# Kernel optimization log

Measured on AMD Instinct MI355X. Metric: run time of the kernel, lower is better.

Reference implementation:

```python
import jax, jax.numpy as jnp
import numpy as np

D = 256
EXP = 4


def layer_norm(x, gamma, beta, eps=1e-5):
    mu = jnp.mean(x, axis=-1, keepdims=True)
    var = jnp.var(x, axis=-1, keepdims=True)
    return (x - mu) / jnp.sqrt(var + eps) * gamma + beta


def setup_inputs() -> dict:
    key = jax.random.key(0)
    ks = jax.random.split(key, 7)
    B, N = 8, 2048
    x = jax.random.normal(ks[0], (B, N, D), dtype=jnp.float32)
    w1 = jax.random.normal(ks[1], (D, EXP * D), dtype=jnp.float32) * (1.0 / np.sqrt(D))
    b1 = jnp.zeros((EXP * D,), dtype=jnp.float32)
    w2 = jax.random.normal(ks[2], (EXP * D, D), dtype=jnp.float32) * (1.0 / np.sqrt(EXP * D))
    b2 = jnp.zeros((D,), dtype=jnp.float32)
    g1 = jnp.ones((D,), dtype=jnp.float32)
    be1 = jnp.zeros((D,), dtype=jnp.float32)
    g2 = jnp.ones((D,), dtype=jnp.float32)
    be2 = jnp.zeros((D,), dtype=jnp.float32)
    return {"x": x, "w1": w1, "b1": b1, "w2": w2, "b2": b2,
            "gamma1": g1, "beta1": be1, "gamma2": g2, "beta2": be2}


def reference(x, w1, b1, w2, b2, gamma1, beta1, gamma2, beta2):
    # Sublayer 1: x + SA(LN(x)); SA uses raw QK^T softmax with Q=K=V=LN(x)
    h = layer_norm(x, gamma1, beta1)               # [B,N,D]
    scale = jnp.sqrt(jnp.float32(h.shape[-1]))
    scores = jnp.einsum('bnd,bmd->bnm', h, h) / scale  # [B,N,N]
    prob = jax.nn.softmax(scores, axis=-1)
    sa_out = jnp.einsum('bnm,bmd->bnd', prob, h)
    x = x + sa_out
    # Sublayer 2: x + FFN(LN(x))
    h2 = layer_norm(x, gamma2, beta2)
    ffn = jax.nn.relu(h2 @ w1 + b1) @ w2 + b2
    return x + ffn
```

## Files before the change

kernel.cpp:

```cpp
#include <hip/hip_runtime.h>
#include <hip/hip_bf16.h>

typedef unsigned short u16;
typedef unsigned int u32;
typedef __attribute__((ext_vector_type(8))) short short8;
typedef __attribute__((ext_vector_type(4))) short short4v;
typedef __attribute__((ext_vector_type(4))) float f32x4;

typedef unsigned int __attribute__((address_space(1))) as1_u32;
typedef unsigned int __attribute__((address_space(3))) as3_u32;

__device__ __forceinline__ void gload16(const void* g, void* l) {
    __builtin_amdgcn_global_load_lds((const as1_u32*)g, (as3_u32*)l, 16, 0, 0);
}

__device__ __forceinline__ u16 f2b(float f) {
    union { float f; unsigned u; } v; v.f = f;
    unsigned r = v.u + 0x7fffu + ((v.u >> 16) & 1u);
    return (u16)(r >> 16);
}

__device__ __forceinline__ f32x4 mfma32(short8 a, short8 b, f32x4 c) {
    return __builtin_amdgcn_mfma_f32_16x16x32_bf16(a, b, c, 0, 0, 0);
}
__device__ __forceinline__ f32x4 mfma16(short4v a, short4v b, f32x4 c) {
    asm("v_mfma_f32_16x16x16_bf16 %0, %1, %2, %0" : "+v"(c) : "v"(a), "v"(b));
    return c;
}

__global__ void transpose_cast(const float* __restrict__ src,
                               u16* __restrict__ dst, int R, int C) {
    __shared__ float tile[32][33];
    const int c0 = blockIdx.x * 32, r0 = blockIdx.y * 32;
    const int tx = threadIdx.x, ty = threadIdx.y;
#pragma unroll
    for (int i = ty; i < 32; i += 8)
        tile[i][tx] = src[(size_t)(r0 + i) * C + c0 + tx];
    __syncthreads();
#pragma unroll
    for (int i = ty; i < 32; i += 8)
        dst[(size_t)(c0 + i) * R + r0 + tx] = f2b(tile[tx][i]);
}

__global__ void transpose_bf16(const u16* __restrict__ src, u16* __restrict__ dst) {
    __shared__ u16 t[32][33];
    const int b = blockIdx.z;
    const int n0 = blockIdx.x * 32, d0 = blockIdx.y * 32;
    const int tx = threadIdx.x, ty = threadIdx.y;
    const u16* s = src + (size_t)b * (2048 * 256);
    u16* d = dst + (size_t)b * (2048 * 256);
#pragma unroll
    for (int i = ty; i < 32; i += 8)
        t[i][tx] = s[(size_t)(n0 + i) * 256 + d0 + tx];
    __syncthreads();
#pragma unroll
    for (int i = ty; i < 32; i += 8)
        d[(size_t)(d0 + i) * 2048 + n0 + tx] = t[tx][i];
}

__global__ __launch_bounds__(256) void ln_kernel(
    const float* __restrict__ x, const float* __restrict__ g,
    const float* __restrict__ be, u16* __restrict__ out) {
    const int lane = threadIdx.x & 63;
    const size_t row = (size_t)blockIdx.x * 4 + (threadIdx.x >> 6);
    const float4 v = *((const float4*)(x + row * 256) + lane);
    float s  = v.x + v.y + v.z + v.w;
    float s2 = v.x * v.x + v.y * v.y + v.z * v.z + v.w * v.w;
#pragma unroll
    for (int m = 1; m < 64; m <<= 1) {
        s  += __shfl_xor(s, m);
        s2 += __shfl_xor(s2, m);
    }
    const float mean = s * (1.0f / 256.0f);
    const float var  = s2 * (1.0f / 256.0f) - mean * mean;
    const float rstd = rsqrtf(var + 1e-5f);
    const float4 gv = *((const float4*)g + lane);
    const float4 bv = *((const float4*)be + lane);
    ushort4 o;
    o.x = f2b((v.x - mean) * rstd * gv.x + bv.x);
    o.y = f2b((v.y - mean) * rstd * gv.y + bv.y);
    o.z = f2b((v.z - mean) * rstd * gv.z + bv.z);
    o.w = f2b((v.w - mean) * rstd * gv.w + bv.w);
    *((ushort4*)(out + row * 256) + lane) = o;
}

#define ATTN_LDS_BYTES (2*65536 + 2048)

__global__ __launch_bounds__(512, 2) void attn_kernel(
    const u16* __restrict__ h, const u16* __restrict__ hT,
    const float* __restrict__ x, float* __restrict__ xmid) {
    extern __shared__ char smem[];
    const int tid  = threadIdx.x;
    const int w    = tid >> 6;
    const int lane = tid & 63;
    const int grp  = lane >> 4;
    const int l16  = lane & 15;
    const int kvq  = w & 3;
    const int qh   = w >> 2;
    const int bid  = blockIdx.x;
    const int b    = bid & 7;
    const int q0   = (bid >> 3) * 64;

    const u16* hb = h + (size_t)b * (2048 * 256);
    const char* hbB = (const char*)hb;
    const char* hTB = (const char*)(hT + (size_t)b * (2048 * 256));

    short8 qf[2][8];
#pragma unroll
    for (int st = 0; st < 2; ++st) {
        const u16* qp = hb + (size_t)(q0 + qh * 32 + st * 16 + l16) * 256 + grp * 8;
#pragma unroll
        for (int kk = 0; kk < 8; ++kk) qf[st][kk] = *(const short8*)(qp + kk * 32);
    }

    f32x4 oacc[2][16];
#pragma unroll
    for (int st = 0; st < 2; ++st)
#pragma unroll
        for (int dt = 0; dt < 16; ++dt) oacc[st][dt] = (f32x4){0.f, 0.f, 0.f, 0.f};
    float m_run[2] = {-1e30f, -1e30f};
    float l_run[2] = {0.f, 0.f};

    const char* gK0 = hbB + ((size_t)(tid >> 5) << 9)
                          + (((tid & 31) ^ ((tid >> 5) & 7)) << 4);
    const char* gV0 = hTB + ((size_t)(tid >> 3) << 12)
                          + (((tid & 7) ^ ((tid >> 3) & 7)) << 4);

    {
        char* lK = smem + w * 1024;
        char* lV = smem + 32768 + w * 1024;
#pragma unroll
        for (int it = 0; it < 4; ++it) gload16(gK0 + (size_t)it * 8192, lK + it * 8192);
#pragma unroll
        for (int it = 0; it < 4; ++it) gload16(gV0 + (size_t)it * 262144, lV + it * 8192);
    }
    __syncthreads();

    for (int kt = 0; kt < 32; ++kt) {
        const int cur = kt & 1;
        if (kt < 31) {
            char* lK = smem + (cur ^ 1) * 65536 + w * 1024;
            char* lV = smem + (cur ^ 1) * 65536 + 32768 + w * 1024;
            const char* gK = gK0 + (size_t)(kt + 1) * 32768;
            const char* gV = gV0 + (size_t)(kt + 1) * 128;
#pragma unroll
            for (int it = 0; it < 4; ++it) gload16(gK + (size_t)it * 8192, lK + it * 8192);
#pragma unroll
            for (int it = 0; it < 4; ++it) gload16(gV + (size_t)it * 262144, lV + it * 8192);
        }
        const char* KB = smem + cur * 65536;
        const char* VB = KB + 32768;

        f32x4 sacc[2] = {(f32x4){0.f,0.f,0.f,0.f}, (f32x4){0.f,0.f,0.f,0.f}};
        const char* rb = KB + ((kvq * 16 + l16) << 9);
#pragma unroll
        for (int kk = 0; kk < 8; ++kk) {
            const int c = grp + 4 * kk;
            const int swz = (c & ~7) | ((c ^ l16) & 7);
            const short8 kf = *(const short8*)(rb + (swz << 4));
            sacc[0] = mfma32(kf, qf[0][kk], sacc[0]);
            sacc[1] = mfma32(kf, qf[1][kk], sacc[1]);
        }

        short4v pa[2];
#pragma unroll
        for (int st = 0; st < 2; ++st) {
            float p0 = sacc[st][0] * 0.0625f, p1 = sacc[st][1] * 0.0625f;
            float p2 = sacc[st][2] * 0.0625f, p3 = sacc[st][3] * 0.0625f;
            float mx = fmaxf(fmaxf(p0, p1), fmaxf(p2, p3));
            mx = fmaxf(mx, __shfl_xor(mx, 16));
            mx = fmaxf(mx, __shfl_xor(mx, 32));
            if (__any(mx > m_run[st] + 8.f)) {
                const float mnew  = fmaxf(m_run[st], mx);
                const float alpha = __expf(m_run[st] - mnew);
                m_run[st] = mnew;
                l_run[st] *= alpha;
                float ar[4];
#pragma unroll
                for (int r = 0; r < 4; ++r) ar[r] = __shfl(alpha, grp * 4 + r);
#pragma unroll
                for (int dt = 0; dt < 16; ++dt)
#pragma unroll
                    for (int r = 0; r < 4; ++r) oacc[st][dt][r] *= ar[r];
            }
            const float e0 = __expf(p0 - m_run[st]);
            const float e1 = __expf(p1 - m_run[st]);
            const float e2 = __expf(p2 - m_run[st]);
            const float e3 = __expf(p3 - m_run[st]);
            float lt = e0 + e1 + e2 + e3;
            lt += __shfl_xor(lt, 16);
            lt += __shfl_xor(lt, 32);
            l_run[st] += lt;
            pa[st] = (short4v){(short)f2b(e0), (short)f2b(e1),
                               (short)f2b(e2), (short)f2b(e3)};
        }

        const char* vbase = VB + l16 * 128
                          + (((kvq * 2 + (grp >> 1)) ^ (l16 & 7)) << 4)
                          + (grp & 1) * 8;
#pragma unroll
        for (int dt = 0; dt < 16; ++dt) {
            const short4v bv = *(const short4v*)(vbase + dt * 2048);
            oacc[0][dt] = mfma16(pa[0], bv, oacc[0][dt]);
            oacc[1][dt] = mfma16(pa[1], bv, oacc[1][dt]);
        }
        __syncthreads();
    }

    float2* ml = (float2*)(smem + 131072);
    if (lane < 16) {
        float2 t0; t0.x = m_run[0]; t0.y = l_run[0];
        float2 t1; t1.x = m_run[1]; t1.y = l_run[1];
        ml[w * 32 + lane]      = t0;
        ml[w * 32 + 16 + lane] = t1;
    }
    const int dq = w & 3;
    float an[2][4][4];
    const float* xb = x + (size_t)b * (2048 * 256);
    float* ob = xmid + (size_t)b * (2048 * 256);
#pragma unroll
    for (int rnd = 0; rnd < 2; ++rnd) {
        char* wb = smem + w * 16384;
#pragma unroll
        for (int st = 0; st < 2; ++st)
#pragma unroll
            for (int k = 0; k < 8; ++k)
                *(f32x4*)(wb + ((st * 8 + k) * 64 + lane) * 16) = oacc[st][rnd * 8 + k];
        __syncthreads();
        if (rnd == 0) {
#pragma unroll
            for (int st = 0; st < 2; ++st)
#pragma unroll
                for (int rr = 0; rr < 4; ++rr) {
                    const int q = st * 16 + grp * 4 + rr;
                    float mv[4], lv[4];
#pragma unroll
                    for (int kq = 0; kq < 4; ++kq) {
                        const float2 t = ml[(qh * 4 + kq) * 32 + q];
                        mv[kq] = t.x; lv[kq] = t.y;
                    }
                    const float M = fmaxf(fmaxf(mv[0], mv[1]), fmaxf(mv[2], mv[3]));
                    float a[4], L = 0.f;
#pragma unroll
                    for (int kq = 0; kq < 4; ++kq) {
                        a[kq] = __expf(mv[kq] - M);
                        L += a[kq] * lv[kq];
                    }
                    const float inv = 1.0f / L;
#pragma unroll
                    for (int kq = 0; kq < 4; ++kq) an[st][rr][kq] = a[kq] * inv;
                }
        }
#pragma unroll
        for (int j = 0; j < 2; ++j) {
            const int dtg = rnd * 8 + dq * 2 + j;
#pragma unroll
            for (int st = 0; st < 2; ++st) {
                f32x4 acc = (f32x4){0.f, 0.f, 0.f, 0.f};
#pragma unroll
                for (int kq = 0; kq < 4; ++kq) {
                    const f32x4 ch = *(const f32x4*)(smem + (qh * 4 + kq) * 16384
                                     + ((st * 8 + dq * 2 + j) * 64 + lane) * 16);
#pragma unroll
                    for (int rr = 0; rr < 4; ++rr) acc[rr] += an[st][rr][kq] * ch[rr];
                }
                const int col = dtg * 16 + l16;
#pragma unroll
                for (int rr = 0; rr < 4; ++rr) {
                    const int row = q0 + qh * 32 + st * 16 + grp * 4 + rr;
                    const size_t idx = (size_t)row * 256 + col;
                    ob[idx] = xb[idx] + acc[rr];
                }
            }
        }
        if (rnd == 0) __syncthreads();
    }
}

#define FFN_LDS_BYTES (2*65536 + 4096)

__global__ __launch_bounds__(512, 2) void ffn_kernel(
    const u16* __restrict__ h2, const u16* __restrict__ w1t,
    const u16* __restrict__ w2t, const float* __restrict__ b1,
    const float* __restrict__ b2, float* __restrict__ xmid) {
    extern __shared__ char smem[];
    const int tid  = threadIdx.x;
    const int w    = tid >> 6;
    const int lane = tid & 63;
    const int grp  = lane >> 4;
    const int l16  = lane & 15;
    const int hq   = w & 3;
    const int th   = w >> 2;
    const int t0   = blockIdx.x * 64;
    char* b1lds = smem + 131072;

    short8 af[2][8];
#pragma unroll
    for (int st = 0; st < 2; ++st) {
        const u16* ap = h2 + (size_t)(t0 + th * 32 + st * 16 + l16) * 256 + grp * 8;
#pragma unroll
        for (int kk = 0; kk < 8; ++kk) af[st][kk] = *(const short8*)(ap + kk * 32);
    }

    f32x4 oacc[2][16];
#pragma unroll
    for (int st = 0; st < 2; ++st)
#pragma unroll
        for (int dt = 0; dt < 16; ++dt) oacc[st][dt] = (f32x4){0.f, 0.f, 0.f, 0.f};

    const char* g10 = (const char*)w1t + ((size_t)(tid >> 5) << 9)
                                       + (((tid & 31) ^ ((tid >> 5) & 7)) << 4);
    const char* g20 = (const char*)w2t + ((size_t)(tid >> 3) << 11)
                                       + (((tid & 7) ^ ((tid >> 3) & 7)) << 4);

    {
        char* l1 = smem + w * 1024;
        char* l2 = smem + 32768 + w * 1024;
#pragma unroll
        for (int it = 0; it < 4; ++it) gload16(g10 + (size_t)it * 8192, l1 + it * 8192);
#pragma unroll
        for (int it = 0; it < 4; ++it) gload16(g20 + (size_t)it * 131072, l2 + it * 8192);
        if (tid < 256) gload16((const char*)b1 + tid * 16, b1lds + tid * 16);
    }
    __syncthreads();

    for (int hc = 0; hc < 16; ++hc) {
        const int cur = hc & 1;
        if (hc < 15) {
            char* l1 = smem + (cur ^ 1) * 65536 + w * 1024;
            char* l2 = smem + (cur ^ 1) * 65536 + 32768 + w * 1024;
            const char* g1 = g10 + (size_t)(hc + 1) * 32768;
            const char* g2 = g20 + (size_t)(hc + 1) * 128;
#pragma unroll
            for (int it = 0; it < 4; ++it) gload16(g1 + (size_t)it * 8192, l1 + it * 8192);
#pragma unroll
            for (int it = 0; it < 4; ++it) gload16(g2 + (size_t)it * 131072, l2 + it * 8192);
        }
        const char* W1B = smem + cur * 65536;
        const char* W2B = W1B + 32768;

        f32x4 sacc[2] = {(f32x4){0.f,0.f,0.f,0.f}, (f32x4){0.f,0.f,0.f,0.f}};
        const char* rb = W1B + ((hq * 16 + l16) << 9);
#pragma unroll
        for (int kk = 0; kk < 8; ++kk) {
            const int c = grp + 4 * kk;
            const int swz = (c & ~7) | ((c ^ l16) & 7);
            const short8 wf = *(const short8*)(rb + (swz << 4));
            sacc[0] = mfma32(wf, af[0][kk], sacc[0]);
            sacc[1] = mfma32(wf, af[1][kk], sacc[1]);
        }

        const f32x4 bb = *(const f32x4*)(b1lds + (hc * 64 + hq * 16 + grp * 4) * 4);
        short4v pa[2];
#pragma unroll
        for (int st = 0; st < 2; ++st) {
            const float v0 = fmaxf(sacc[st][0] + bb[0], 0.f);
            const float v1 = fmaxf(sacc[st][1] + bb[1], 0.f);
            const float v2 = fmaxf(sacc[st][2] + bb[2], 0.f);
            const float v3 = fmaxf(sacc[st][3] + bb[3], 0.f);
            pa[st] = (short4v){(short)f2b(v0), (short)f2b(v1),
                               (short)f2b(v2), (short)f2b(v3)};
        }

        const char* vbase = W2B + l16 * 128
                          + (((hq * 2 + (grp >> 1)) ^ (l16 & 7)) << 4)
                          + (grp & 1) * 8;
#pragma unroll
        for (int dt = 0; dt < 16; ++dt) {
            const short4v bv = *(const short4v*)(vbase + dt * 2048);
            oacc[0][dt] = mfma16(pa[0], bv, oacc[0][dt]);
            oacc[1][dt] = mfma16(pa[1], bv, oacc[1][dt]);
        }
        __syncthreads();
    }

    const int dq = w & 3;
#pragma unroll
    for (int rnd = 0; rnd < 2; ++rnd) {
        char* wb = smem + w * 16384;
#pragma unroll
        for (int st = 0; st < 2; ++st)
#pragma unroll
            for (int k = 0; k < 8; ++k)
                *(f32x4*)(wb + ((st * 8 + k) * 64 + lane) * 16) = oacc[st][rnd * 8 + k];
        __syncthreads();
#pragma unroll
        for (int j = 0; j < 2; ++j) {
            const int dtg = rnd * 8 + dq * 2 + j;
            const int col = dtg * 16 + l16;
            const float b2v = b2[col];
#pragma unroll
            for (int st = 0; st < 2; ++st) {
                f32x4 acc = (f32x4){0.f, 0.f, 0.f, 0.f};
#pragma unroll
                for (int kq = 0; kq < 4; ++kq) {
                    const f32x4 ch = *(const f32x4*)(smem + (th * 4 + kq) * 16384
                                     + ((st * 8 + dq * 2 + j) * 64 + lane) * 16);
#pragma unroll
                    for (int rr = 0; rr < 4; ++rr) acc[rr] += ch[rr];
                }
#pragma unroll
                for (int rr = 0; rr < 4; ++rr) {
                    const int row = t0 + th * 32 + st * 16 + grp * 4 + rr;
                    const size_t idx = (size_t)row * 256 + col;
                    xmid[idx] = xmid[idx] + acc[rr] + b2v;
                }
            }
        }
        if (rnd == 0) __syncthreads();
    }
}

extern "C" void kernel_launch(void* const* d_in, const int* in_sizes, int n_in,
                              void* d_out, int out_size, void* d_ws, size_t ws_size,
                              hipStream_t stream) {
    (void)in_sizes; (void)n_in; (void)out_size; (void)ws_size;
    const float* x   = (const float*)d_in[0];
    const float* w1  = (const float*)d_in[1];
    const float* b1  = (const float*)d_in[2];
    const float* w2  = (const float*)d_in[3];
    const float* b2  = (const float*)d_in[4];
    const float* g1  = (const float*)d_in[5];
    const float* be1 = (const float*)d_in[6];
    const float* g2  = (const float*)d_in[7];
    const float* be2 = (const float*)d_in[8];
    float* out = (float*)d_out;

    char* ws = (char*)d_ws;
    u16* h   = (u16*)ws;
    u16* hT  = (u16*)(ws + 8388608);
    u16* w1t = (u16*)(ws + 16777216);
    u16* w2t = (u16*)(ws + 17301504);

    hipFuncSetAttribute((const void*)attn_kernel,
                        hipFuncAttributeMaxDynamicSharedMemorySize, ATTN_LDS_BYTES);
    hipFuncSetAttribute((const void*)ffn_kernel,
                        hipFuncAttributeMaxDynamicSharedMemorySize, FFN_LDS_BYTES);

    transpose_cast<<<dim3(32, 8), dim3(32, 8), 0, stream>>>(w1, w1t, 256, 1024);
    transpose_cast<<<dim3(8, 32), dim3(32, 8), 0, stream>>>(w2, w2t, 1024, 256);

    ln_kernel<<<4096, 256, 0, stream>>>(x, g1, be1, h);
    transpose_bf16<<<dim3(64, 8, 8), dim3(32, 8), 0, stream>>>(h, hT);
    attn_kernel<<<256, 512, ATTN_LDS_BYTES, stream>>>(h, hT, x, out);

    ln_kernel<<<4096, 256, 0, stream>>>(out, g2, be2, h);
    ffn_kernel<<<256, 512, FFN_LDS_BYTES, stream>>>(h, w1t, w2t, b1, b2, out);
}
```

Baseline: 199.0 us.

## Pre-pack V and W2 into MFMA-ready tiled layout with contiguous loads and setprio

Replaces the plain transposes of h and W2 with packing kernels that write each 64-row tile as a contiguous, pre-swizzled 32KB block. Attention and FFN kernels can then stream V/W2 tiles with contiguous 16-byte global-to-LDS loads instead of strided ones. They also read one short8 per lane to feed two 16x16x16 MFMAs, halving the LDS read count. s_setprio is raised around the MFMA loops to favour matrix issue across waves. This adds more intricate index arithmetic in the packers, which could introduce layout bugs.

```diff
diff --git a/kernel.cpp b/kernel.cpp
--- a/kernel.cpp
+++ b/kernel.cpp
@@ -42,20 +42,58 @@
         dst[(size_t)(c0 + i) * R + r0 + tx] = f2b(tile[tx][i]);
 }
 
-__global__ void transpose_bf16(const u16* __restrict__ src, u16* __restrict__ dst) {
+__global__ void pack_v(const u16* __restrict__ h, u16* __restrict__ hV) {
     __shared__ u16 t[32][33];
     const int b = blockIdx.z;
     const int n0 = blockIdx.x * 32, d0 = blockIdx.y * 32;
     const int tx = threadIdx.x, ty = threadIdx.y;
-    const u16* s = src + (size_t)b * (2048 * 256);
-    u16* d = dst + (size_t)b * (2048 * 256);
+    const u16* s = h + (size_t)b * (2048 * 256);
 #pragma unroll
     for (int i = ty; i < 32; i += 8)
         t[i][tx] = s[(size_t)(n0 + i) * 256 + d0 + tx];
     __syncthreads();
+    const int tid = ty * 32 + tx;
+    if (tid < 128) {
+        const int kvc = tid & 7, dl = tid >> 3;
+        short8 vv;
+#pragma unroll
+        for (int e = 0; e < 4; ++e) {
+            vv[e]     = (short)t[kvc * 4 + e][dl];
+            vv[4 + e] = (short)t[kvc * 4 + e][dl + 16];
+        }
+        const int kt   = n0 >> 6;
+        const int kv4  = ((n0 & 32) >> 2) + kvc;
+        const int slot = (d0 >> 5) ^ (dl & 7);
+        char* dst = (char*)hV + ((size_t)b * 32 + kt) * 32768
+                  + (kv4 * 16 + dl) * 128 + slot * 16;
+        *(short8*)dst = vv;
+    }
+}
+
+__global__ void pack_w2(const float* __restrict__ w2, u16* __restrict__ w2p) {
+    __shared__ float t[32][33];
+    const int h0 = blockIdx.x * 32, d0 = blockIdx.y * 32;
+    const int tx = threadIdx.x, ty = threadIdx.y;
 #pragma unroll
     for (int i = ty; i < 32; i += 8)
-        d[(size_t)(d0 + i) * 2048 + n0 + tx] = t[tx][i];
+        t[i][tx] = w2[(size_t)(h0 + i) * 256 + d0 + tx];
+    __syncthreads();
+    const int tid = ty * 32 + tx;
+    if (tid < 128) {
+        const int hc4 = tid & 7, dl = tid >> 3;
+        short8 vv;
+#pragma unroll
+        for (int e = 0; e < 4; ++e) {
+            vv[e]     = (short)f2b(t[hc4 * 4 + e][dl]);
+            vv[4 + e] = (short)f2b(t[hc4 * 4 + e][dl + 16]);
+        }
+        const int hc   = h0 >> 6;
+        const int h4   = ((h0 & 32) >> 2) + hc4;
+        const int slot = (d0 >> 5) ^ (dl & 7);
+        char* dst = (char*)w2p + (size_t)hc * 32768
+                  + (h4 * 16 + dl) * 128 + slot * 16;
+        *(short8*)dst = vv;
+    }
 }
 
 __global__ __launch_bounds__(256) void ln_kernel(
@@ -87,7 +125,7 @@
 #define ATTN_LDS_BYTES (2*65536 + 2048)
 
 __global__ __launch_bounds__(512, 2) void attn_kernel(
-    const u16* __restrict__ h, const u16* __restrict__ hT,
+    const u16* __restrict__ h, const u16* __restrict__ hV,
     const float* __restrict__ x, float* __restrict__ xmid) {
     extern __shared__ char smem[];
     const int tid  = threadIdx.x;
@@ -103,7 +141,7 @@
 
     const u16* hb = h + (size_t)b * (2048 * 256);
     const char* hbB = (const char*)hb;
-    const char* hTB = (const char*)(hT + (size_t)b * (2048 * 256));
+    const char* hVB = (const char*)hV + (size_t)b * 1048576;
 
     short8 qf[2][8];
 #pragma unroll
@@ -123,8 +161,7 @@
 
     const char* gK0 = hbB + ((size_t)(tid >> 5) << 9)
                           + (((tid & 31) ^ ((tid >> 5) & 7)) << 4);
-    const char* gV0 = hTB + ((size_t)(tid >> 3) << 12)
-                          + (((tid & 7) ^ ((tid >> 3) & 7)) << 4);
+    const char* gV0 = hVB + tid * 16;
 
     {
         char* lK = smem + w * 1024;
@@ -132,7 +169,7 @@
 #pragma unroll
         for (int it = 0; it < 4; ++it) gload16(gK0 + (size_t)it * 8192, lK + it * 8192);
 #pragma unroll
-        for (int it = 0; it < 4; ++it) gload16(gV0 + (size_t)it * 262144, lV + it * 8192);
+        for (int it = 0; it < 4; ++it) gload16(gV0 + (size_t)it * 8192, lV + it * 8192);
     }
     __syncthreads();
 
@@ -142,17 +179,18 @@
             char* lK = smem + (cur ^ 1) * 65536 + w * 1024;
             char* lV = smem + (cur ^ 1) * 65536 + 32768 + w * 1024;
             const char* gK = gK0 + (size_t)(kt + 1) * 32768;
-            const char* gV = gV0 + (size_t)(kt + 1) * 128;
+            const char* gV = gV0 + (size_t)(kt + 1) * 32768;
 #pragma unroll
             for (int it = 0; it < 4; ++it) gload16(gK + (size_t)it * 8192, lK + it * 8192);
 #pragma unroll
-            for (int it = 0; it < 4; ++it) gload16(gV + (size_t)it * 262144, lV + it * 8192);
+            for (int it = 0; it < 4; ++it) gload16(gV + (size_t)it * 8192, lV + it * 8192);
         }
         const char* KB = smem + cur * 65536;
         const char* VB = KB + 32768;
 
         f32x4 sacc[2] = {(f32x4){0.f,0.f,0.f,0.f}, (f32x4){0.f,0.f,0.f,0.f}};
         const char* rb = KB + ((kvq * 16 + l16) << 9);
+        __builtin_amdgcn_s_setprio(1);
 #pragma unroll
         for (int kk = 0; kk < 8; ++kk) {
             const int c = grp + 4 * kk;
@@ -161,6 +199,7 @@
             sacc[0] = mfma32(kf, qf[0][kk], sacc[0]);
             sacc[1] = mfma32(kf, qf[1][kk], sacc[1]);
         }
+        __builtin_amdgcn_s_setprio(0);
 
         short4v pa[2];
 #pragma unroll
@@ -195,15 +234,20 @@
                                (short)f2b(e2), (short)f2b(e3)};
         }
 
-        const char* vbase = VB + l16 * 128
-                          + (((kvq * 2 + (grp >> 1)) ^ (l16 & 7)) << 4)
-                          + (grp & 1) * 8;
-#pragma unroll
-        for (int dt = 0; dt < 16; ++dt) {
-            const short4v bv = *(const short4v*)(vbase + dt * 2048);
-            oacc[0][dt] = mfma16(pa[0], bv, oacc[0][dt]);
-            oacc[1][dt] = mfma16(pa[1], bv, oacc[1][dt]);
-        }
+        const char* vbase = VB + ((kvq * 4 + grp) * 16 + l16) * 128;
+        const int sx = l16 & 7;
+        __builtin_amdgcn_s_setprio(1);
+#pragma unroll
+        for (int dt2 = 0; dt2 < 8; ++dt2) {
+            const short8 vv = *(const short8*)(vbase + ((dt2 ^ sx) << 4));
+            const short4v lo = __builtin_shufflevector(vv, vv, 0, 1, 2, 3);
+            const short4v hi = __builtin_shufflevector(vv, vv, 4, 5, 6, 7);
+            oacc[0][2 * dt2]     = mfma16(pa[0], lo, oacc[0][2 * dt2]);
+            oacc[0][2 * dt2 + 1] = mfma16(pa[0], hi, oacc[0][2 * dt2 + 1]);
+            oacc[1][2 * dt2]     = mfma16(pa[1], lo, oacc[1][2 * dt2]);
+            oacc[1][2 * dt2 + 1] = mfma16(pa[1], hi, oacc[1][2 * dt2 + 1]);
+        }
+        __builtin_amdgcn_s_setprio(0);
         __syncthreads();
     }
 
@@ -281,7 +325,7 @@
 
 __global__ __launch_bounds__(512, 2) void ffn_kernel(
     const u16* __restrict__ h2, const u16* __restrict__ w1t,
-    const u16* __restrict__ w2t, const float* __restrict__ b1,
+    const u16* __restrict__ w2p, const float* __restrict__ b1,
     const float* __restrict__ b2, float* __restrict__ xmid) {
     extern __shared__ char smem[];
     const int tid  = threadIdx.x;
@@ -310,8 +354,7 @@
 
     const char* g10 = (const char*)w1t + ((size_t)(tid >> 5) << 9)
                                        + (((tid & 31) ^ ((tid >> 5) & 7)) << 4);
-    const char* g20 = (const char*)w2t + ((size_t)(tid >> 3) << 11)
-                                       + (((tid & 7) ^ ((tid >> 3) & 7)) << 4);
+    const char* g20 = (const char*)w2p + tid * 16;
 
     {
         char* l1 = smem + w * 1024;
@@ -319,7 +362,7 @@
 #pragma unroll
         for (int it = 0; it < 4; ++it) gload16(g10 + (size_t)it * 8192, l1 + it * 8192);
 #pragma unroll
-        for (int it = 0; it < 4; ++it) gload16(g20 + (size_t)it * 131072, l2 + it * 8192);
+        for (int it = 0; it < 4; ++it) gload16(g20 + (size_t)it * 8192, l2 + it * 8192);
         if (tid < 256) gload16((const char*)b1 + tid * 16, b1lds + tid * 16);
     }
     __syncthreads();
@@ -330,17 +373,18 @@
             char* l1 = smem + (cur ^ 1) * 65536 + w * 1024;
             char* l2 = smem + (cur ^ 1) * 65536 + 32768 + w * 1024;
             const char* g1 = g10 + (size_t)(hc + 1) * 32768;
-            const char* g2 = g20 + (size_t)(hc + 1) * 128;
+            const char* g2 = g20 + (size_t)(hc + 1) * 32768;
 #pragma unroll
             for (int it = 0; it < 4; ++it) gload16(g1 + (size_t)it * 8192, l1 + it * 8192);
 #pragma unroll
-            for (int it = 0; it < 4; ++it) gload16(g2 + (size_t)it * 131072, l2 + it * 8192);
+            for (int it = 0; it < 4; ++it) gload16(g2 + (size_t)it * 8192, l2 + it * 8192);
         }
         const char* W1B = smem + cur * 65536;
         const char* W2B = W1B + 32768;
 
         f32x4 sacc[2] = {(f32x4){0.f,0.f,0.f,0.f}, (f32x4){0.f,0.f,0.f,0.f}};
         const char* rb = W1B + ((hq * 16 + l16) << 9);
+        __builtin_amdgcn_s_setprio(1);
 #pragma unroll
         for (int kk = 0; kk < 8; ++kk) {
             const int c = grp + 4 * kk;
@@ -349,6 +393,7 @@
             sacc[0] = mfma32(wf, af[0][kk], sacc[0]);
             sacc[1] = mfma32(wf, af[1][kk], sacc[1]);
         }
+        __builtin_amdgcn_s_setprio(0);
 
         const f32x4 bb = *(const f32x4*)(b1lds + (hc * 64 + hq * 16 + grp * 4) * 4);
         short4v pa[2];
@@ -362,15 +407,20 @@
                                (short)f2b(v2), (short)f2b(v3)};
         }
 
-        const char* vbase = W2B + l16 * 128
-                          + (((hq * 2 + (grp >> 1)) ^ (l16 & 7)) << 4)
-                          + (grp & 1) * 8;
-#pragma unroll
-        for (int dt = 0; dt < 16; ++dt) {
-            const short4v bv = *(const short4v*)(vbase + dt * 2048);
-            oacc[0][dt] = mfma16(pa[0], bv, oacc[0][dt]);
-            oacc[1][dt] = mfma16(pa[1], bv, oacc[1][dt]);
-        }
+        const char* vbase = W2B + ((hq * 4 + grp) * 16 + l16) * 128;
+        const int sx = l16 & 7;
+        __builtin_amdgcn_s_setprio(1);
+#pragma unroll
+        for (int dt2 = 0; dt2 < 8; ++dt2) {
+            const short8 vv = *(const short8*)(vbase + ((dt2 ^ sx) << 4));
+            const short4v lo = __builtin_shufflevector(vv, vv, 0, 1, 2, 3);
+            const short4v hi = __builtin_shufflevector(vv, vv, 4, 5, 6, 7);
+            oacc[0][2 * dt2]     = mfma16(pa[0], lo, oacc[0][2 * dt2]);
+            oacc[0][2 * dt2 + 1] = mfma16(pa[0], hi, oacc[0][2 * dt2 + 1]);
+            oacc[1][2 * dt2]     = mfma16(pa[1], lo, oacc[1][2 * dt2]);
+            oacc[1][2 * dt2 + 1] = mfma16(pa[1], hi, oacc[1][2 * dt2 + 1]);
+        }
+        __builtin_amdgcn_s_setprio(0);
         __syncthreads();
     }
 
@@ -428,9 +478,9 @@
 
     char* ws = (char*)d_ws;
     u16* h   = (u16*)ws;
-    u16* hT  = (u16*)(ws + 8388608);
+    u16* hV  = (u16*)(ws + 8388608);
     u16* w1t = (u16*)(ws + 16777216);
-    u16* w2t = (u16*)(ws + 17301504);
+    u16* w2p = (u16*)(ws + 17301504);
 
     hipFuncSetAttribute((const void*)attn_kernel,
                         hipFuncAttributeMaxDynamicSharedMemorySize, ATTN_LDS_BYTES);
@@ -438,12 +488,12 @@
                         hipFuncAttributeMaxDynamicSharedMemorySize, FFN_LDS_BYTES);
 
     transpose_cast<<<dim3(32, 8), dim3(32, 8), 0, stream>>>(w1, w1t, 256, 1024);
-    transpose_cast<<<dim3(8, 32), dim3(32, 8), 0, stream>>>(w2, w2t, 1024, 256);
+    pack_w2<<<dim3(32, 8), dim3(32, 8), 0, stream>>>(w2, w2p);
 
     ln_kernel<<<4096, 256, 0, stream>>>(x, g1, be1, h);
-    transpose_bf16<<<dim3(64, 8, 8), dim3(32, 8), 0, stream>>>(h, hT);
-    attn_kernel<<<256, 512, ATTN_LDS_BYTES, stream>>>(h, hT, x, out);
+    pack_v<<<dim3(64, 8, 8), dim3(32, 8), 0, stream>>>(h, hV);
+    attn_kernel<<<256, 512, ATTN_LDS_BYTES, stream>>>(h, hV, x, out);
 
     ln_kernel<<<4096, 256, 0, stream>>>(out, g2, be2, h);
-    ffn_kernel<<<256, 512, FFN_LDS_BYTES, stream>>>(h, w1t, w2t, b1, b2, out);
-}
+    ffn_kernel<<<256, 512, FFN_LDS_BYTES, stream>>>(h, w1t, w2p, b1, b2, out);
+}
```

Result: no change. 199.2 us (+0.1%).
